# Kernel tuning notes

Hardware: AMD Instinct MI355X
Metric: run time of the kernel (lower is better)

## Reference

```python
import jax, jax.numpy as jnp
import numpy as np

TOP_K = 2

def setup_inputs() -> dict:
    key = jax.random.key(0)
    k1, k2 = jax.random.split(key)
    hidden_states = jax.random.normal(k1, (4, 4096, 4096), dtype=jnp.float32)
    # nn.Linear(dim, num_experts, bias=False) weight: [num_experts, dim]
    router_weight = jax.random.normal(k2, (64, 4096), dtype=jnp.float32) * (4096 ** -0.5)
    return {"hidden_states": hidden_states, "router_weight": router_weight}

def reference(hidden_states, router_weight):
    # logits: (batch, seq, num_experts)
    logits = jnp.einsum('bsd,ed->bse', hidden_states, router_weight)
    # Shazeer et al. 2017 Eq. 1: softmax over the kept top-k logits.
    topk_logits, topk_indices = jax.lax.top_k(logits, TOP_K)
    topk_scores = jax.nn.softmax(topk_logits, axis=-1)  # (batch, seq, top_k)
    return topk_scores, topk_indices
```

## Files before the change

### kernel.cpp

```cpp
#include <hip/hip_runtime.h>
#include <math.h>

#define TOKENS 16384
#define DIM    4096
#define NEXP   64
#define KSPLIT 4
#define KSLICE (DIM / KSPLIT)
#define BK     32
#define NCHUNK (KSLICE / BK)
#define NCHUNK_G (DIM / BK)

typedef _Float16 f16x8 __attribute__((ext_vector_type(8)));
typedef float    f32x4 __attribute__((ext_vector_type(4)));

#define MFMA16(a, b, c) __builtin_amdgcn_mfma_f32_16x16x32_f16((a), (b), (c), 0, 0, 0)

__global__ __launch_bounds__(256)
void pack_w_kernel(const float* __restrict__ w, uint4* __restrict__ wpk) {
    const int lane = threadIdx.x & 63;
    const int t    = threadIdx.x >> 6;
    const int c    = blockIdx.x;
    const int e    = 16 * t + (lane & 15);
    const int k0   = 32 * c + 8 * (lane >> 4);

    const float* src = w + (size_t)e * DIM + k0;
    const float4 v0 = *(const float4*)(src);
    const float4 v1 = *(const float4*)(src + 4);
    const float xs[8] = {v0.x, v0.y, v0.z, v0.w, v1.x, v1.y, v1.z, v1.w};

    f16x8 hi, lo;
#pragma unroll
    for (int j = 0; j < 8; ++j) {
        const float xv = xs[j];
        _Float16 h = (_Float16)xv;
        float hf = (float)h;
        if (fabsf(xv) < 6.103515625e-05f) {
            h = (_Float16)0.f; hf = 0.f;
        }
        hi[j] = h;
        lo[j] = (_Float16)((xv - hf) * 65536.f);
    }

    uint4* dst = wpk + ((size_t)(c * 4 + t) * 64 + lane) * 2;
    dst[0] = *(const uint4*)&hi;
    dst[1] = *(const uint4*)&lo;
}

__device__ __forceinline__ void split_a(const float4 lo, const float4 hi,
                                        f16x8& ah, f16x8& al) {
    const float xs[8] = {lo.x, lo.y, lo.z, lo.w, hi.x, hi.y, hi.z, hi.w};
#pragma unroll
    for (int j = 0; j < 8; ++j) {
        const float xv = xs[j];
        const _Float16 h = (_Float16)xv;
        ah[j] = h;
        al[j] = (_Float16)((xv - (float)h) * 65536.f);
    }
}

__device__ __forceinline__ void fma3(const f16x8 ah, const f16x8 al,
                                     const f16x8 bh, const f16x8 bl,
                                     f32x4& a1, f32x4& a2) {
    a1 = MFMA16(ah, bh, a1);
    a2 = MFMA16(ah, bl, a2);
    a2 = MFMA16(al, bh, a2);
}

__global__ __launch_bounds__(256)
__attribute__((amdgpu_waves_per_eu(4, 4)))
void router_gemm_kernel(const float* __restrict__ x,
                        const f16x8* __restrict__ wpk,
                        float* __restrict__ part) {
    const int tid    = threadIdx.x;
    const int lane   = tid & 63;
    const int wv     = tid >> 6;
    const int bid    = blockIdx.x;
    const int ks     = bid & (KSPLIT - 1);
    const int tb     = bid >> 2;
    const int token0 = tb * 64 + wv * 16;

    const int row = token0 + (lane & 15);
    const float* xp = x + (size_t)row * DIM + ks * KSLICE + 8 * (lane >> 4);

    const f16x8* bp = wpk + (size_t)ks * NCHUNK * 512 + lane * 2;

    f32x4 a10, a11, a12, a13, a20, a21, a22, a23;
    const f32x4 zero = {0.f, 0.f, 0.f, 0.f};
    a10 = a11 = a12 = a13 = zero;
    a20 = a21 = a22 = a23 = zero;

    float4 xAlo = *(const float4*)(xp);
    float4 xAhi = *(const float4*)(xp + 4);
    float4 xBlo = *(const float4*)(xp + BK);
    float4 xBhi = *(const float4*)(xp + BK + 4);
    f16x8 bh0 = bp[0],   bl0 = bp[1];
    f16x8 bh1 = bp[128], bl1 = bp[129];
    f16x8 bh2 = bp[256], bl2 = bp[257];
    f16x8 bh3 = bp[384], bl3 = bp[385];

    f16x8 ah, al;
#pragma unroll 1
    for (int c = 0; c < NCHUNK; c += 2) {
        split_a(xAlo, xAhi, ah, al);
        {
            const int cn = (c + 2 < NCHUNK) ? c + 2 : 0;
            xAlo = *(const float4*)(xp + cn * BK);
            xAhi = *(const float4*)(xp + cn * BK + 4);
        }
        fma3(ah, al, bh0, bl0, a10, a20);
        fma3(ah, al, bh1, bl1, a11, a21);
        {
            const f16x8* pn = bp + (size_t)(c + 1) * 512;
            bh0 = pn[0]; bl0 = pn[1]; bh1 = pn[128]; bl1 = pn[129];
        }
        fma3(ah, al, bh2, bl2, a12, a22);
        fma3(ah, al, bh3, bl3, a13, a23);
        {
            const f16x8* pn = bp + (size_t)(c + 1) * 512;
            bh2 = pn[256]; bl2 = pn[257]; bh3 = pn[384]; bl3 = pn[385];
        }
        split_a(xBlo, xBhi, ah, al);
        {
            const int cn = (c + 3 < NCHUNK) ? c + 3 : 0;
            xBlo = *(const float4*)(xp + cn * BK);
            xBhi = *(const float4*)(xp + cn * BK + 4);
        }
        fma3(ah, al, bh0, bl0, a10, a20);
        fma3(ah, al, bh1, bl1, a11, a21);
        {
            const f16x8* pn = bp + (size_t)(c + 2) * 512;
            bh0 = pn[0]; bl0 = pn[1]; bh1 = pn[128]; bl1 = pn[129];
        }
        fma3(ah, al, bh2, bl2, a12, a22);
        fma3(ah, al, bh3, bl3, a13, a23);
        {
            const f16x8* pn = bp + (size_t)(c + 2) * 512;
            bh2 = pn[256]; bl2 = pn[257]; bh3 = pn[384]; bl3 = pn[385];
        }
    }

    float* pout = part + ((size_t)ks * TOKENS + token0 + 4 * (lane >> 4)) * NEXP
                + (lane & 15);
    const f32x4 v0 = a10 + a20 * (1.f / 65536.f);
    const f32x4 v1 = a11 + a21 * (1.f / 65536.f);
    const f32x4 v2 = a12 + a22 * (1.f / 65536.f);
    const f32x4 v3 = a13 + a23 * (1.f / 65536.f);
#pragma unroll
    for (int r = 0; r < 4; ++r) {
        pout[(size_t)r * NEXP +  0] = v0[r];
        pout[(size_t)r * NEXP + 16] = v1[r];
        pout[(size_t)r * NEXP + 32] = v2[r];
        pout[(size_t)r * NEXP + 48] = v3[r];
    }
}

__global__ __launch_bounds__(256)
void topk_kernel(const float* __restrict__ part, float* __restrict__ out) {
    const int lane  = threadIdx.x & 63;
    const int wv    = threadIdx.x >> 6;
    const int token = blockIdx.x * 4 + wv;

    float logit = 0.f;
#pragma unroll
    for (int s = 0; s < KSPLIT; ++s)
        logit += part[((size_t)s * TOKENS + token) * NEXP + lane];

    float v1 = logit; int i1 = lane;
#pragma unroll
    for (int off = 32; off > 0; off >>= 1) {
        const float ov = __shfl_xor(v1, off);
        const int   oi = __shfl_xor(i1, off);
        if (ov > v1 || (ov == v1 && oi < i1)) { v1 = ov; i1 = oi; }
    }
    float v2 = (lane == i1) ? -INFINITY : logit; int i2 = lane;
#pragma unroll
    for (int off = 32; off > 0; off >>= 1) {
        const float ov = __shfl_xor(v2, off);
        const int   oi = __shfl_xor(i2, off);
        if (ov > v2 || (ov == v2 && oi < i2)) { v2 = ov; i2 = oi; }
    }

    if (lane == 0) {
        const float e = expf(v2 - v1);
        const float r = 1.f / (1.f + e);
        out[2 * token + 0] = r;
        out[2 * token + 1] = e * r;
        out[2 * TOKENS + 2 * token + 0] = (float)i1;
        out[2 * TOKENS + 2 * token + 1] = (float)i2;
    }
}

extern "C" void kernel_launch(void* const* d_in, const int* in_sizes, int n_in,
                              void* d_out, int out_size, void* d_ws, size_t ws_size,
                              hipStream_t stream) {
    const float* x = (const float*)d_in[0];
    const float* w = (const float*)d_in[1];
    float* out  = (float*)d_out;
    float* part = (float*)d_ws;
    uint4* wpk = (uint4*)((char*)d_ws + (size_t)KSPLIT * TOKENS * NEXP * sizeof(float));

    pack_w_kernel<<<NCHUNK_G, 256, 0, stream>>>(w, wpk);
    router_gemm_kernel<<<(TOKENS / 64) * KSPLIT, 256, 0, stream>>>(
        x, (const f16x8*)wpk, part);
    topk_kernel<<<TOKENS / 4, 256, 0, stream>>>(part, out);
}
```

Before: 420.8 us.

## Stage X and packed W tiles into LDS via global_load_lds double buffering

Replaces the per-lane register prefetch of X and packed weights with direct global-to-LDS async loads, double-buffered per chunk and using an XOR-swizzled layout for the X tile. The weight chunk is now loaded once per block and shared across the four waves instead of each wave reading all of it, and the packed-weight layout is changed to match. In exchange it adds two barriers per chunk and the LDS round trip, and prefetching only one chunk ahead may expose HBM latency on this memory-bound GEMM.

```diff
diff --git a/kernel.cpp b/kernel.cpp
--- a/kernel.cpp
+++ b/kernel.cpp
@@ -14,6 +14,12 @@
 typedef float    f32x4 __attribute__((ext_vector_type(4)));
 
 #define MFMA16(a, b, c) __builtin_amdgcn_mfma_f32_16x16x32_f16((a), (b), (c), 0, 0, 0)
+
+__device__ __forceinline__ void gload16(const void* g, void* l) {
+    __builtin_amdgcn_global_load_lds(
+        (const __attribute__((address_space(1))) void*)g,
+        (__attribute__((address_space(3))) void*)l, 16, 0, 0);
+}
 
 __global__ __launch_bounds__(256)
 void pack_w_kernel(const float* __restrict__ w, uint4* __restrict__ wpk) {
@@ -41,14 +47,13 @@
         lo[j] = (_Float16)((xv - hf) * 65536.f);
     }
 
-    uint4* dst = wpk + ((size_t)(c * 4 + t) * 64 + lane) * 2;
-    dst[0] = *(const uint4*)&hi;
-    dst[1] = *(const uint4*)&lo;
-}
-
-__device__ __forceinline__ void split_a(const float4 lo, const float4 hi,
+    wpk[(size_t)c * 512 + (2 * t + 0) * 64 + lane] = *(const uint4*)&hi;
+    wpk[(size_t)c * 512 + (2 * t + 1) * 64 + lane] = *(const uint4*)&lo;
+}
+
+__device__ __forceinline__ void split_a(const f32x4 lo, const f32x4 hi,
                                         f16x8& ah, f16x8& al) {
-    const float xs[8] = {lo.x, lo.y, lo.z, lo.w, hi.x, hi.y, hi.z, hi.w};
+    const float xs[8] = {lo[0], lo[1], lo[2], lo[3], hi[0], hi[1], hi[2], hi[3]};
 #pragma unroll
     for (int j = 0; j < 8; ++j) {
         const float xv = xs[j];
@@ -69,88 +74,89 @@
 __global__ __launch_bounds__(256)
 __attribute__((amdgpu_waves_per_eu(4, 4)))
 void router_gemm_kernel(const float* __restrict__ x,
-                        const f16x8* __restrict__ wpk,
+                        const uint4* __restrict__ wpk,
                         float* __restrict__ part) {
-    const int tid    = threadIdx.x;
-    const int lane   = tid & 63;
-    const int wv     = tid >> 6;
-    const int bid    = blockIdx.x;
-    const int ks     = bid & (KSPLIT - 1);
-    const int tb     = bid >> 2;
-    const int token0 = tb * 64 + wv * 16;
-
-    const int row = token0 + (lane & 15);
-    const float* xp = x + (size_t)row * DIM + ks * KSLICE + 8 * (lane >> 4);
-
-    const f16x8* bp = wpk + (size_t)ks * NCHUNK * 512 + lane * 2;
+    __shared__ uint4 lds[2048];
+
+    const int tid  = threadIdx.x;
+    const int lane = tid & 63;
+    const int wv   = tid >> 6;
+    const int bid  = blockIdx.x;
+    const int ks   = bid & (KSPLIT - 1);
+    const int tb   = bid >> 2;
+    const int wt0  = tb * 64 + wv * 16;
+
+    const int rl = lane >> 3;
+    const int sb = (lane & 7) ^ rl;
+    const float* xsrc0 = x + (size_t)(wt0 + rl)     * DIM + ks * KSLICE + 4 * sb;
+    const float* xsrc1 = x + (size_t)(wt0 + 8 + rl) * DIM + ks * KSLICE + 4 * sb;
+    const uint4* bsrc = wpk + (size_t)(ks * NCHUNK) * 512 + (2 * wv) * 64 + lane;
+
+    const int r  = lane & 15;
+    const int kb = 2 * (lane >> 4);
+    const int xi0 = r * 8 + ((kb    ) ^ (r & 7));
+    const int xi1 = r * 8 + ((kb + 1) ^ (r & 7));
 
     f32x4 a10, a11, a12, a13, a20, a21, a22, a23;
     const f32x4 zero = {0.f, 0.f, 0.f, 0.f};
     a10 = a11 = a12 = a13 = zero;
     a20 = a21 = a22 = a23 = zero;
 
-    float4 xAlo = *(const float4*)(xp);
-    float4 xAhi = *(const float4*)(xp + 4);
-    float4 xBlo = *(const float4*)(xp + BK);
-    float4 xBhi = *(const float4*)(xp + BK + 4);
-    f16x8 bh0 = bp[0],   bl0 = bp[1];
-    f16x8 bh1 = bp[128], bl1 = bp[129];
-    f16x8 bh2 = bp[256], bl2 = bp[257];
-    f16x8 bh3 = bp[384], bl3 = bp[385];
-
-    f16x8 ah, al;
+    auto STAGE = [&](int cc, int bsel) {
+        uint4* Xb = &lds[bsel * 1024 + wv * 128];
+        uint4* Bb = &lds[bsel * 1024 + 512 + (2 * wv) * 64];
+        gload16(xsrc0 + cc * BK,            Xb);
+        gload16(xsrc1 + cc * BK,            Xb + 64);
+        gload16(bsrc + (size_t)cc * 512,      Bb);
+        gload16(bsrc + (size_t)cc * 512 + 64, Bb + 64);
+    };
+
+    STAGE(0, 0);
+
 #pragma unroll 1
-    for (int c = 0; c < NCHUNK; c += 2) {
-        split_a(xAlo, xAhi, ah, al);
-        {
-            const int cn = (c + 2 < NCHUNK) ? c + 2 : 0;
-            xAlo = *(const float4*)(xp + cn * BK);
-            xAhi = *(const float4*)(xp + cn * BK + 4);
-        }
+    for (int c = 0; c < NCHUNK; ++c) {
+        STAGE((c + 1) & (NCHUNK - 1), (c + 1) & 1);
+
+        asm volatile("s_waitcnt vmcnt(4)" ::: "memory");
+        __builtin_amdgcn_s_barrier();
+
+        const uint4* Xr = &lds[(c & 1) * 1024 + wv * 128];
+        const uint4* Br = &lds[(c & 1) * 1024 + 512];
+
+        const f32x4 xlo = *(const f32x4*)&Xr[xi0];
+        const f32x4 xhi = *(const f32x4*)&Xr[xi1];
+        const f16x8 bh0 = *(const f16x8*)&Br[0 * 64 + lane];
+        const f16x8 bl0 = *(const f16x8*)&Br[1 * 64 + lane];
+        const f16x8 bh1 = *(const f16x8*)&Br[2 * 64 + lane];
+        const f16x8 bl1 = *(const f16x8*)&Br[3 * 64 + lane];
+        const f16x8 bh2 = *(const f16x8*)&Br[4 * 64 + lane];
+        const f16x8 bl2 = *(const f16x8*)&Br[5 * 64 + lane];
+        const f16x8 bh3 = *(const f16x8*)&Br[6 * 64 + lane];
+        const f16x8 bl3 = *(const f16x8*)&Br[7 * 64 + lane];
+
+        f16x8 ah, al;
+        split_a(xlo, xhi, ah, al);
         fma3(ah, al, bh0, bl0, a10, a20);
         fma3(ah, al, bh1, bl1, a11, a21);
-        {
-            const f16x8* pn = bp + (size_t)(c + 1) * 512;
-            bh0 = pn[0]; bl0 = pn[1]; bh1 = pn[128]; bl1 = pn[129];
-        }
         fma3(ah, al, bh2, bl2, a12, a22);
         fma3(ah, al, bh3, bl3, a13, a23);
-        {
-            const f16x8* pn = bp + (size_t)(c + 1) * 512;
-            bh2 = pn[256]; bl2 = pn[257]; bh3 = pn[384]; bl3 = pn[385];
-        }
-        split_a(xBlo, xBhi, ah, al);
-        {
-            const int cn = (c + 3 < NCHUNK) ? c + 3 : 0;
-            xBlo = *(const float4*)(xp + cn * BK);
-            xBhi = *(const float4*)(xp + cn * BK + 4);
-        }
-        fma3(ah, al, bh0, bl0, a10, a20);
-        fma3(ah, al, bh1, bl1, a11, a21);
-        {
-            const f16x8* pn = bp + (size_t)(c + 2) * 512;
-            bh0 = pn[0]; bl0 = pn[1]; bh1 = pn[128]; bl1 = pn[129];
-        }
-        fma3(ah, al, bh2, bl2, a12, a22);
-        fma3(ah, al, bh3, bl3, a13, a23);
-        {
-            const f16x8* pn = bp + (size_t)(c + 2) * 512;
-            bh2 = pn[256]; bl2 = pn[257]; bh3 = pn[384]; bl3 = pn[385];
-        }
-    }
-
-    float* pout = part + ((size_t)ks * TOKENS + token0 + 4 * (lane >> 4)) * NEXP
+
+        asm volatile("s_waitcnt lgkmcnt(0)" ::: "memory");
+        __builtin_amdgcn_s_barrier();
+    }
+
+    float* pout = part + ((size_t)ks * TOKENS + wt0 + 4 * (lane >> 4)) * NEXP
                 + (lane & 15);
     const f32x4 v0 = a10 + a20 * (1.f / 65536.f);
     const f32x4 v1 = a11 + a21 * (1.f / 65536.f);
     const f32x4 v2 = a12 + a22 * (1.f / 65536.f);
     const f32x4 v3 = a13 + a23 * (1.f / 65536.f);
 #pragma unroll
-    for (int r = 0; r < 4; ++r) {
-        pout[(size_t)r * NEXP +  0] = v0[r];
-        pout[(size_t)r * NEXP + 16] = v1[r];
-        pout[(size_t)r * NEXP + 32] = v2[r];
-        pout[(size_t)r * NEXP + 48] = v3[r];
+    for (int rr = 0; rr < 4; ++rr) {
+        pout[(size_t)rr * NEXP +  0] = v0[rr];
+        pout[(size_t)rr * NEXP + 16] = v1[rr];
+        pout[(size_t)rr * NEXP + 32] = v2[rr];
+        pout[(size_t)rr * NEXP + 48] = v3[rr];
     }
 }
 
@@ -200,7 +206,6 @@
     uint4* wpk = (uint4*)((char*)d_ws + (size_t)KSPLIT * TOKENS * NEXP * sizeof(float));
 
     pack_w_kernel<<<NCHUNK_G, 256, 0, stream>>>(w, wpk);
-    router_gemm_kernel<<<(TOKENS / 64) * KSPLIT, 256, 0, stream>>>(
-        x, (const f16x8*)wpk, part);
+    router_gemm_kernel<<<(TOKENS / 64) * KSPLIT, 256, 0, stream>>>(x, wpk, part);
     topk_kernel<<<TOKENS / 4, 256, 0, stream>>>(part, out);
 }
```

Measured after the change: 380.3 us. -9.6%, faster.
